# Kernel tuning notes

Hardware: AMD Instinct MI355X
Metric: run time of the kernel (lower is better)

Reference implementation:

```python
import jax, jax.numpy as jnp
import numpy as np

NUM_GROUPS = 32
EPS = 1e-6


def group_norm(x, w, b):
    # x: (B, C, L); normalize per group of C//32 channels over (channels-in-group, L)
    B, C, L = x.shape
    xg = x.reshape(B, NUM_GROUPS, C // NUM_GROUPS, L)
    mean = jnp.mean(xg, axis=(2, 3), keepdims=True)
    var = jnp.var(xg, axis=(2, 3), keepdims=True)
    xn = ((xg - mean) * jax.lax.rsqrt(var + EPS)).reshape(B, C, L)
    return xn * w[None, :, None] + b[None, :, None]


def conv1x1(x, w, b):
    # 1x1 Conv1d == channel-mixing linear. x: (B,C,L), w: (O,C), b: (O,)
    return jnp.einsum('oc,bcl->bol', w, x) + b[None, :, None]


def setup_inputs() -> dict:
    key = jax.random.key(0)
    ks = jax.random.split(key, 6)
    B, C, L = 8, 512, 2048
    s = 1.0 / np.sqrt(C)
    return {
        'x': jax.random.normal(ks[0], (B, C, L), dtype=jnp.float32),
        'gn_w': jnp.ones((C,), jnp.float32),
        'gn_b': jnp.zeros((C,), jnp.float32),
        'wq': jax.random.normal(ks[1], (C, C), dtype=jnp.float32) * s,
        'bq': jnp.zeros((C,), jnp.float32),
        'wk': jax.random.normal(ks[2], (C, C), dtype=jnp.float32) * s,
        'bk': jnp.zeros((C,), jnp.float32),
        'wv': jax.random.normal(ks[3], (C, C), dtype=jnp.float32) * s,
        'bv': jnp.zeros((C,), jnp.float32),
        'wo': jax.random.normal(ks[4], (C, C), dtype=jnp.float32) * s,
        'bo': jnp.zeros((C,), jnp.float32),
    }


def reference(x, gn_w, gn_b, wq, bq, wk, bk, wv, bv, wo, bo):
    B, C, L = x.shape
    h = group_norm(x, gn_w, gn_b)
    q = conv1x1(h, wq, bq)  # (B,C,L)
    k = conv1x1(h, wk, bk)
    v = conv1x1(h, wv, bv)
    scale = jnp.asarray(C, x.dtype) ** -0.5
    # scores over length: w[b,i,j] = sum_c q[b,c,i] k[b,c,j]
    w_ = jnp.einsum('bci,bcj->bij', q, k) * scale
    w_ = jax.nn.softmax(w_, axis=-1)
    # h[b,c,i] = sum_j w[b,i,j] v[b,c,j]
    h = jnp.einsum('bij,bcj->bci', w_, v)
    h = conv1x1(h, wo, bo)
    return x + h
```

## Files before the change

kernel.cpp:

```cpp
#include <hip/hip_runtime.h>
#include <math.h>

#define BATCH 8
#define CH 512
#define LEN 2048
#define NG 32
#define CPG 16

typedef unsigned short u16;
typedef __bf16 bf16x8 __attribute__((ext_vector_type(8)));
typedef float f32x16 __attribute__((ext_vector_type(16)));

__device__ __forceinline__ u16 f2bf(float f) {
    union { float f; unsigned u; } c; c.f = f;
    unsigned r = c.u + 0x7fffu + ((c.u >> 16) & 1u);
    return (u16)(r >> 16);
}
__device__ __forceinline__ float bf2f(u16 h) {
    union { unsigned u; float f; } c; c.u = ((unsigned)h) << 16;
    return c.f;
}
__device__ __forceinline__ void gload16(const u16* g, u16* l) {
    __builtin_amdgcn_global_load_lds(
        (const __attribute__((address_space(1))) unsigned int*)g,
        (__attribute__((address_space(3))) unsigned int*)l, 16, 0, 0);
}

__global__ __launch_bounds__(256) void zerof4(float4* __restrict__ p) {
    p[blockIdx.x * 256 + threadIdx.x] = make_float4(0.f, 0.f, 0.f, 0.f);
}

__global__ __launch_bounds__(256) void wconv4(const float* __restrict__ w0, const float* __restrict__ w1,
                                              const float* __restrict__ w2, const float* __restrict__ w3,
                                              u16* __restrict__ o0, u16* __restrict__ o1,
                                              u16* __restrict__ o2, u16* __restrict__ o3) {
    const float* s; u16* d;
    switch (blockIdx.y) {
        case 0: s = w0; d = o0; break;
        case 1: s = w1; d = o1; break;
        case 2: s = w2; d = o2; break;
        default: s = w3; d = o3; break;
    }
    const int i = blockIdx.x * 256 + threadIdx.x;
    float4 f = ((const float4*)s)[i];
    ushort4 o = make_ushort4(f2bf(f.x), f2bf(f.y), f2bf(f.z), f2bf(f.w));
    ((ushort4*)d)[i] = o;
}

__global__ __launch_bounds__(256) void gn_stats(const float* __restrict__ x,
                                                const float* __restrict__ gw,
                                                const float* __restrict__ gb,
                                                float* __restrict__ gnA,
                                                float* __restrict__ gnB) {
    const int b = blockIdx.x >> 5, g = blockIdx.x & 31;
    const float4* xp = (const float4*)(x + ((size_t)b * CH + (size_t)g * CPG) * LEN);
    float s = 0.f, s2 = 0.f;
    for (int i = threadIdx.x; i < (CPG * LEN) / 4; i += 256) {
        float4 v = xp[i];
        s += v.x + v.y + v.z + v.w;
        s2 = fmaf(v.x, v.x, fmaf(v.y, v.y, fmaf(v.z, v.z, fmaf(v.w, v.w, s2))));
    }
    #pragma unroll
    for (int off = 32; off > 0; off >>= 1) {
        s  += __shfl_down(s, off, 64);
        s2 += __shfl_down(s2, off, 64);
    }
    __shared__ float sm[2][4];
    const int lane = threadIdx.x & 63, wv = threadIdx.x >> 6;
    if (lane == 0) { sm[0][wv] = s; sm[1][wv] = s2; }
    __syncthreads();
    if (threadIdx.x < CPG) {
        const float S  = sm[0][0] + sm[0][1] + sm[0][2] + sm[0][3];
        const float S2 = sm[1][0] + sm[1][1] + sm[1][2] + sm[1][3];
        const float mean = S * (1.f / (CPG * LEN));
        const float var  = S2 * (1.f / (CPG * LEN)) - mean * mean;
        const float rstd = rsqrtf(var + 1e-6f);
        const int c = g * CPG + threadIdx.x;
        const float sc = rstd * gw[c];
        gnA[b * CH + c] = sc;
        gnB[b * CH + c] = gb[c] - mean * sc;
    }
}

__global__ __launch_bounds__(256) void gn_apply_t(const float* __restrict__ x,
                                                  const float* __restrict__ gnA,
                                                  const float* __restrict__ gnB,
                                                  u16* __restrict__ Ht) {
    __shared__ float tile[64][65];
    const int b = blockIdx.z, c0 = blockIdx.y * 64, l0 = blockIdx.x * 64;
    const int t = threadIdx.x, tl = t & 63, tr = t >> 6;
    #pragma unroll 4
    for (int i = 0; i < 16; ++i) {
        const int c = tr + i * 4;
        const float a = gnA[b * CH + c0 + c];
        const float sh = gnB[b * CH + c0 + c];
        tile[c][tl] = x[((size_t)b * CH + c0 + c) * LEN + l0 + tl] * a + sh;
    }
    __syncthreads();
    #pragma unroll 4
    for (int i = 0; i < 16; ++i) {
        const int l = tr + i * 4;
        Ht[((size_t)b * LEN + l0 + l) * CH + c0 + tl] = f2bf(tile[tl][l]);
    }
}

#define EPI_QK   0
#define EPI_TBN  1
#define EPI_EXP  2
#define EPI_TNRM 3
#define EPI_FIN  4

template <int MODE>
__global__ __launch_bounds__(256) void gemm_bt(
    const u16* __restrict__ A, int lda, long long sA,
    const u16* __restrict__ B, int ldb, long long sB,
    void* __restrict__ Out, void* __restrict__ Out2,
    int ldo, long long sO,
    const float* __restrict__ bias, const float* __restrict__ bias2,
    const float* __restrict__ res, long long sR,
    float* __restrict__ rsum, long long sRS,
    int K, float alpha) {
    __shared__ u16 As[128 * 64];
    __shared__ u16 Bs[128 * 64];
    const int b = blockIdx.z;
    const int n0 = blockIdx.x * 128, m0 = blockIdx.y * 128;
    A += (size_t)b * sA;
    B += (size_t)b * sB;
    const int t = threadIdx.x;
    const int lane = t & 63, wid = t >> 6;

    const int rowL = t >> 3, kq = (t & 7) ^ (rowL & 7);
    const u16* gA[4];
    const u16* gB[4];
    u16* lA[4];
    u16* lB[4];
    #pragma unroll
    for (int g = 0; g < 4; ++g) {
        gA[g] = A + (size_t)(m0 + rowL + g * 32) * lda + kq * 8;
        gB[g] = B + (size_t)(n0 + rowL + g * 32) * ldb + kq * 8;
        lA[g] = As + t * 8 + g * 2048;
        lB[g] = Bs + t * 8 + g * 2048;
    }

    f32x16 acc[2][2];
    #pragma unroll
    for (int i = 0; i < 2; ++i)
        #pragma unroll
        for (int j = 0; j < 2; ++j)
            acc[i][j] = (f32x16)(0.f);

    const int col = lane & 31, half = lane >> 5;
    const int wm = (wid & 1) * 64, wn = (wid >> 1) * 64;
    const int mf = wm + col, nf = wn + col;
    const int mswz = mf & 7, nswz = nf & 7;

    for (int k0 = 0; k0 < K; k0 += 64) {
        #pragma unroll
        for (int g = 0; g < 4; ++g) {
            gload16(gA[g], lA[g]);
            gload16(gB[g], lB[g]);
            gA[g] += 64; gB[g] += 64;
        }
        __syncthreads();
        #pragma unroll
        for (int ks = 0; ks < 4; ++ks) {
            const int kcA = ((ks * 2 + half) ^ mswz) * 8;
            const int kcB = ((ks * 2 + half) ^ nswz) * 8;
            bf16x8 a0 = *(const bf16x8*)(As + (mf)      * 64 + kcA);
            bf16x8 a1 = *(const bf16x8*)(As + (mf + 32) * 64 + kcA);
            bf16x8 b0 = *(const bf16x8*)(Bs + (nf)      * 64 + kcB);
            bf16x8 b1 = *(const bf16x8*)(Bs + (nf + 32) * 64 + kcB);
            acc[0][0] = __builtin_amdgcn_mfma_f32_32x32x16_bf16(a0, b0, acc[0][0], 0, 0, 0);
            acc[0][1] = __builtin_amdgcn_mfma_f32_32x32x16_bf16(a0, b1, acc[0][1], 0, 0, 0);
            acc[1][0] = __builtin_amdgcn_mfma_f32_32x32x16_bf16(a1, b0, acc[1][0], 0, 0, 0);
            acc[1][1] = __builtin_amdgcn_mfma_f32_32x32x16_bf16(a1, b1, acc[1][1], 0, 0, 0);
        }
        __syncthreads();
    }

    if (MODE == EPI_FIN) {
        float* O = (float*)Out + (size_t)b * sO;
        const float* R = res + (size_t)b * sR;
        #pragma unroll
        for (int im = 0; im < 2; ++im)
            #pragma unroll
            for (int g4 = 0; g4 < 4; ++g4) {
                const int mb = m0 + wm + im * 32 + g4 * 8 + half * 4;
                #pragma unroll
                for (int jn = 0; jn < 2; ++jn) {
                    const int n = n0 + wn + jn * 32 + col;
                    const float bb = bias[n];
                    const size_t base = (size_t)n * ldo + mb;
                    const float4 r4 = *(const float4*)&R[base];
                    float4 o4;
                    o4.x = acc[im][jn][g4 * 4 + 0] + bb + r4.x;
                    o4.y = acc[im][jn][g4 * 4 + 1] + bb + r4.y;
                    o4.z = acc[im][jn][g4 * 4 + 2] + bb + r4.z;
                    o4.w = acc[im][jn][g4 * 4 + 3] + bb + r4.w;
                    *(float4*)&O[base] = o4;
                }
            }
    } else if (MODE == EPI_EXP) {
        u16* O = (u16*)Out + (size_t)b * sO;
        float* RS = rsum + (size_t)b * sRS;
        float psum[2] = {0.f, 0.f};
        #pragma unroll
        for (int im = 0; im < 2; ++im)
            #pragma unroll
            for (int g4 = 0; g4 < 4; ++g4) {
                const int mb = m0 + wm + im * 32 + g4 * 8 + half * 4;
                #pragma unroll
                for (int jn = 0; jn < 2; ++jn) {
                    const int n = n0 + wn + jn * 32 + col;
                    u16 h0 = f2bf(__expf(acc[im][jn][g4 * 4 + 0] * alpha));
                    u16 h1 = f2bf(__expf(acc[im][jn][g4 * 4 + 1] * alpha));
                    u16 h2 = f2bf(__expf(acc[im][jn][g4 * 4 + 2] * alpha));
                    u16 h3 = f2bf(__expf(acc[im][jn][g4 * 4 + 3] * alpha));
                    psum[jn] += bf2f(h0) + bf2f(h1) + bf2f(h2) + bf2f(h3);
                    *(ushort4*)&O[(size_t)n * ldo + mb] = make_ushort4(h0, h1, h2, h3);
                }
            }
        #pragma unroll
        for (int jn = 0; jn < 2; ++jn) psum[jn] += __shfl_xor(psum[jn], 32, 64);
        if (half == 0) {
            #pragma unroll
            for (int jn = 0; jn < 2; ++jn)
                atomicAdd(&RS[n0 + wn + jn * 32 + col], psum[jn]);
        }
    } else {
        u16* O;
        const float* bi = bias;
        const float* RS = (MODE == EPI_TNRM) ? rsum + (size_t)b * sRS : nullptr;
        int mbase = m0 + wm;
        if (MODE == EPI_QK) {
            const bool hi = (m0 & 512) != 0;
            O  = (u16*)(hi ? Out2 : Out) + (size_t)b * sO;
            bi = hi ? bias2 : bias;
            mbase = (m0 & 511) + wm;
        } else {
            O = (u16*)Out + (size_t)b * sO;
        }
        float inv[2];
        if (MODE == EPI_TNRM) {
            inv[0] = 1.f / RS[n0 + wn + col];
            inv[1] = 1.f / RS[n0 + wn + 32 + col];
        }
        #pragma unroll
        for (int im = 0; im < 2; ++im)
            #pragma unroll
            for (int g4 = 0; g4 < 4; ++g4) {
                const int mb = mbase + im * 32 + g4 * 8 + half * 4;
                float4 bm = make_float4(0.f, 0.f, 0.f, 0.f);
                if (MODE == EPI_QK) bm = *(const float4*)&bi[mb];
                #pragma unroll
                for (int jn = 0; jn < 2; ++jn) {
                    const int n = n0 + wn + jn * 32 + col;
                    float v0 = acc[im][jn][g4 * 4 + 0];
                    float v1 = acc[im][jn][g4 * 4 + 1];
                    float v2 = acc[im][jn][g4 * 4 + 2];
                    float v3 = acc[im][jn][g4 * 4 + 3];
                    if (MODE == EPI_QK)  { v0 += bm.x; v1 += bm.y; v2 += bm.z; v3 += bm.w; }
                    if (MODE == EPI_TBN) { const float bb = bi[n]; v0 += bb; v1 += bb; v2 += bb; v3 += bb; }
                    if (MODE == EPI_TNRM) { v0 *= inv[jn]; v1 *= inv[jn]; v2 *= inv[jn]; v3 *= inv[jn]; }
                    ushort4 pk = make_ushort4(f2bf(v0), f2bf(v1), f2bf(v2), f2bf(v3));
                    *(ushort4*)&O[(size_t)n * ldo + mb] = pk;
                }
            }
    }
}

extern "C" void kernel_launch(void* const* d_in, const int* in_sizes, int n_in,
                              void* d_out, int out_size, void* d_ws, size_t ws_size,
                              hipStream_t stream) {
    const float* x    = (const float*)d_in[0];
    const float* gn_w = (const float*)d_in[1];
    const float* gn_b = (const float*)d_in[2];
    const float* wq   = (const float*)d_in[3];
    const float* bq   = (const float*)d_in[4];
    const float* wk   = (const float*)d_in[5];
    const float* bk   = (const float*)d_in[6];
    const float* wv   = (const float*)d_in[7];
    const float* bv   = (const float*)d_in[8];
    const float* wo   = (const float*)d_in[9];
    const float* bo   = (const float*)d_in[10];
    float* out = (float*)d_out;

    char* p = (char*)d_ws;
    const size_t WSZ = (size_t)CH * CH * 2;
    const size_t HSZ = (size_t)BATCH * CH * LEN * 2;
    u16* Wqk = (u16*)p; p += 2 * WSZ;
    u16* Wvb = (u16*)p; p += WSZ;
    u16* Wob = (u16*)p; p += WSZ;
    u16* Ht  = (u16*)p; p += HSZ;
    u16* Qt  = (u16*)p; p += HSZ;
    u16* Kt  = (u16*)p; p += HSZ;
    u16* Vb  = (u16*)p; p += HSZ;
    u16* Sb  = (u16*)p; p += (size_t)BATCH * LEN * LEN * 2;
    float* gnA = (float*)p; p += (size_t)BATCH * CH * 4;
    float* gnB = (float*)p; p += (size_t)BATCH * CH * 4;
    float* rowsum = (float*)p;

    const long long sH = (long long)LEN * CH;
    const long long sV = (long long)CH * LEN;
    const long long sS = (long long)LEN * LEN;
    const float scale = 0.04419417382415922f;

    wconv4<<<dim3(256, 4), 256, 0, stream>>>(wq, wk, wv, wo,
                                             Wqk, Wqk + (size_t)CH * CH, Wvb, Wob);
    gn_stats<<<BATCH * NG, 256, 0, stream>>>(x, gn_w, gn_b, gnA, gnB);
    gn_apply_t<<<dim3(LEN / 64, CH / 64, BATCH), 256, 0, stream>>>(x, gnA, gnB, Ht);
    zerof4<<<BATCH * LEN / 1024, 256, 0, stream>>>((float4*)rowsum);

    gemm_bt<EPI_QK><<<dim3(16, 8, 8), 256, 0, stream>>>(
        Wqk, CH, 0, Ht, CH, sH, Qt, Kt, CH, sH, bq, bk, nullptr, 0, nullptr, 0, CH, 0.f);
    gemm_bt<EPI_TBN><<<dim3(4, 16, 8), 256, 0, stream>>>(
        Ht, CH, sH, Wvb, CH, 0, Vb, nullptr, LEN, sV, bv, nullptr, nullptr, 0, nullptr, 0, CH, 0.f);
    gemm_bt<EPI_EXP><<<dim3(16, 16, 8), 256, 0, stream>>>(
        Kt, CH, sH, Qt, CH, sH, Sb, nullptr, LEN, sS, nullptr, nullptr, nullptr, 0, rowsum, LEN, CH, scale);
    gemm_bt<EPI_TNRM><<<dim3(16, 4, 8), 256, 0, stream>>>(
        Vb, LEN, sV, Sb, LEN, sS, Ht, nullptr, CH, sH, nullptr, nullptr, nullptr, 0, rowsum, LEN, LEN, 0.f);
    gemm_bt<EPI_FIN><<<dim3(4, 16, 8), 256, 0, stream>>>(
        Ht, CH, sH, Wob, CH, 0, out, nullptr, LEN, sV, bo, nullptr, x, sV, nullptr, 0, CH, 0.f);
}
```

Baseline: 299.2 us.

## Replace 128x128 GEMM with double-buffered 256-wide tiles, 8 waves, XCD-aware block remap

Rewrites the shared GEMM kernel to use 512-thread blocks with BMx256 tiles (BM 128 or 256). LDS is double-buffered so the next K-slice is prefetched with global_load_lds while MFMAs run on the current one, and s_setprio is raised around the MFMA bursts. Block indices are permuted round-robin across 8 groups to spread work over the XCDs. Larger tiles raise per-block LDS and register use and cut the number of blocks, which risks lower occupancy and tail imbalance on some of the GEMMs.

```diff
diff --git a/kernel.cpp b/kernel.cpp
--- a/kernel.cpp
+++ b/kernel.cpp
@@ -25,6 +25,12 @@
         (const __attribute__((address_space(1))) unsigned int*)g,
         (__attribute__((address_space(3))) unsigned int*)l, 16, 0, 0);
 }
+
+#define BARRIER() do {                                   \
+    asm volatile("" ::: "memory");                       \
+    __builtin_amdgcn_s_barrier();                        \
+    asm volatile("" ::: "memory");                       \
+} while (0)
 
 __global__ __launch_bounds__(256) void zerof4(float4* __restrict__ p) {
     p[blockIdx.x * 256 + threadIdx.x] = make_float4(0.f, 0.f, 0.f, 0.f);
@@ -110,8 +116,8 @@
 #define EPI_TNRM 3
 #define EPI_FIN  4
 
-template <int MODE>
-__global__ __launch_bounds__(256) void gemm_bt(
+template <int MODE, int BM>
+__global__ __launch_bounds__(512, 2) void gemm256(
     const u16* __restrict__ A, int lda, long long sA,
     const u16* __restrict__ B, int ldb, long long sB,
     void* __restrict__ Out, void* __restrict__ Out2,
@@ -120,69 +126,116 @@
     const float* __restrict__ res, long long sR,
     float* __restrict__ rsum, long long sRS,
     int K, float alpha) {
-    __shared__ u16 As[128 * 64];
-    __shared__ u16 Bs[128 * 64];
-    const int b = blockIdx.z;
-    const int n0 = blockIdx.x * 128, m0 = blockIdx.y * 128;
-    A += (size_t)b * sA;
-    B += (size_t)b * sB;
+    constexpr int MF = BM / 64;
+    constexpr int RA = BM / 64;
+    __shared__ u16 As[2][BM * 64];
+    __shared__ u16 Bs[2][256 * 64];
+
+    const int gx = gridDim.x, gy = gridDim.y;
+    int flat = (blockIdx.z * gy + blockIdx.y) * gx + blockIdx.x;
+    const int nb = gx * gy * (int)gridDim.z;
+    flat = (flat & 7) * (nb >> 3) + (flat >> 3);
+    const int bz = flat / (gx * gy);
+    const int rr = flat - bz * gx * gy;
+    const int by = rr / gx;
+    const int bx = rr - by * gx;
+
+    const int n0 = bx * 256, m0 = by * BM;
+    A += (size_t)bz * sA;
+    B += (size_t)bz * sB;
+
     const int t = threadIdx.x;
     const int lane = t & 63, wid = t >> 6;
-
-    const int rowL = t >> 3, kq = (t & 7) ^ (rowL & 7);
-    const u16* gA[4];
+    const int col = lane & 31, half = lane >> 5;
+    const int wm = (wid >> 2) * (BM / 2), wn = (wid & 3) * 64;
+
+    const int rowL = t >> 3;
+    const int kq = ((t & 7) ^ (rowL & 7)) * 8;
+    const u16* gA[RA];
     const u16* gB[4];
-    u16* lA[4];
-    u16* lB[4];
-    #pragma unroll
-    for (int g = 0; g < 4; ++g) {
-        gA[g] = A + (size_t)(m0 + rowL + g * 32) * lda + kq * 8;
-        gB[g] = B + (size_t)(n0 + rowL + g * 32) * ldb + kq * 8;
-        lA[g] = As + t * 8 + g * 2048;
-        lB[g] = Bs + t * 8 + g * 2048;
-    }
-
-    f32x16 acc[2][2];
-    #pragma unroll
-    for (int i = 0; i < 2; ++i)
-        #pragma unroll
-        for (int j = 0; j < 2; ++j)
-            acc[i][j] = (f32x16)(0.f);
-
-    const int col = lane & 31, half = lane >> 5;
-    const int wm = (wid & 1) * 64, wn = (wid >> 1) * 64;
-    const int mf = wm + col, nf = wn + col;
-    const int mswz = mf & 7, nswz = nf & 7;
-
-    for (int k0 = 0; k0 < K; k0 += 64) {
-        #pragma unroll
-        for (int g = 0; g < 4; ++g) {
-            gload16(gA[g], lA[g]);
-            gload16(gB[g], lB[g]);
-            gA[g] += 64; gB[g] += 64;
+    #pragma unroll
+    for (int r = 0; r < RA; ++r) gA[r] = A + (size_t)(m0 + r * 64 + rowL) * lda + kq;
+    #pragma unroll
+    for (int r = 0; r < 4; ++r)  gB[r] = B + (size_t)(n0 + r * 64 + rowL) * ldb + kq;
+    const int dst = t * 8;
+
+    f32x16 acc[MF][2];
+    #pragma unroll
+    for (int mi = 0; mi < MF; ++mi)
+        #pragma unroll
+        for (int nj = 0; nj < 2; ++nj)
+            acc[mi][nj] = (f32x16)(0.f);
+
+    #pragma unroll
+    for (int r = 0; r < RA; ++r) { gload16(gA[r], &As[0][r * 4096 + dst]); gA[r] += 64; }
+    #pragma unroll
+    for (int r = 0; r < 4; ++r)  { gload16(gB[r], &Bs[0][r * 4096 + dst]); gB[r] += 64; }
+    asm volatile("s_waitcnt vmcnt(0)" ::: "memory");
+    BARRIER();
+
+    const int NT = K >> 6;
+    const int cw8 = col & 7;
+
+    for (int kt = 0; kt < NT; ++kt) {
+        const int cur = kt & 1;
+        const u16* __restrict__ Ab = As[cur];
+        const u16* __restrict__ Bb = Bs[cur];
+        u16* Ad = As[cur ^ 1];
+        u16* Bd = Bs[cur ^ 1];
+        const bool pf = (kt + 1 < NT);
+
+        #pragma unroll
+        for (int p = 0; p < 2; ++p) {
+            const int s0 = ((4 * p + half) ^ cw8) * 8;
+            const int s1 = ((4 * p + 2 + half) ^ cw8) * 8;
+            bf16x8 av[MF][2], bv[2][2];
+            #pragma unroll
+            for (int mi = 0; mi < MF; ++mi) {
+                const u16* base = Ab + (wm + mi * 32 + col) * 64;
+                av[mi][0] = *(const bf16x8*)(base + s0);
+                av[mi][1] = *(const bf16x8*)(base + s1);
+            }
+            #pragma unroll
+            for (int nj = 0; nj < 2; ++nj) {
+                const u16* base = Bb + (wn + nj * 32 + col) * 64;
+                bv[nj][0] = *(const bf16x8*)(base + s0);
+                bv[nj][1] = *(const bf16x8*)(base + s1);
+            }
+            if (pf) {
+                if (p == 0) {
+                    #pragma unroll
+                    for (int r = 0; r < RA / 2; ++r) { gload16(gA[r], Ad + r * 4096 + dst); gA[r] += 64; }
+                    #pragma unroll
+                    for (int r = 0; r < 2; ++r)      { gload16(gB[r], Bd + r * 4096 + dst); gB[r] += 64; }
+                } else {
+                    #pragma unroll
+                    for (int r = RA / 2; r < RA; ++r) { gload16(gA[r], Ad + r * 4096 + dst); gA[r] += 64; }
+                    #pragma unroll
+                    for (int r = 2; r < 4; ++r)       { gload16(gB[r], Bd + r * 4096 + dst); gB[r] += 64; }
+                }
+            }
+            BARRIER();
+            __builtin_amdgcn_s_setprio(1);
+            #pragma unroll
+            for (int h = 0; h < 2; ++h)
+                #pragma unroll
+                for (int mi = 0; mi < MF; ++mi)
+                    #pragma unroll
+                    for (int nj = 0; nj < 2; ++nj)
+                        acc[mi][nj] = __builtin_amdgcn_mfma_f32_32x32x16_bf16(
+                            av[mi][h], bv[nj][h], acc[mi][nj], 0, 0, 0);
+            __builtin_amdgcn_s_setprio(0);
+            if (p == 0) BARRIER();
         }
-        __syncthreads();
-        #pragma unroll
-        for (int ks = 0; ks < 4; ++ks) {
-            const int kcA = ((ks * 2 + half) ^ mswz) * 8;
-            const int kcB = ((ks * 2 + half) ^ nswz) * 8;
-            bf16x8 a0 = *(const bf16x8*)(As + (mf)      * 64 + kcA);
-            bf16x8 a1 = *(const bf16x8*)(As + (mf + 32) * 64 + kcA);
-            bf16x8 b0 = *(const bf16x8*)(Bs + (nf)      * 64 + kcB);
-            bf16x8 b1 = *(const bf16x8*)(Bs + (nf + 32) * 64 + kcB);
-            acc[0][0] = __builtin_amdgcn_mfma_f32_32x32x16_bf16(a0, b0, acc[0][0], 0, 0, 0);
-            acc[0][1] = __builtin_amdgcn_mfma_f32_32x32x16_bf16(a0, b1, acc[0][1], 0, 0, 0);
-            acc[1][0] = __builtin_amdgcn_mfma_f32_32x32x16_bf16(a1, b0, acc[1][0], 0, 0, 0);
-            acc[1][1] = __builtin_amdgcn_mfma_f32_32x32x16_bf16(a1, b1, acc[1][1], 0, 0, 0);
-        }
-        __syncthreads();
+        asm volatile("s_waitcnt vmcnt(0)" ::: "memory");
+        BARRIER();
     }
 
     if (MODE == EPI_FIN) {
-        float* O = (float*)Out + (size_t)b * sO;
-        const float* R = res + (size_t)b * sR;
-        #pragma unroll
-        for (int im = 0; im < 2; ++im)
+        float* O = (float*)Out + (size_t)bz * sO;
+        const float* R = res + (size_t)bz * sR;
+        #pragma unroll
+        for (int im = 0; im < MF; ++im)
             #pragma unroll
             for (int g4 = 0; g4 < 4; ++g4) {
                 const int mb = m0 + wm + im * 32 + g4 * 8 + half * 4;
@@ -201,11 +254,11 @@
                 }
             }
     } else if (MODE == EPI_EXP) {
-        u16* O = (u16*)Out + (size_t)b * sO;
-        float* RS = rsum + (size_t)b * sRS;
+        u16* O = (u16*)Out + (size_t)bz * sO;
+        float* RS = rsum + (size_t)bz * sRS;
         float psum[2] = {0.f, 0.f};
         #pragma unroll
-        for (int im = 0; im < 2; ++im)
+        for (int im = 0; im < MF; ++im)
             #pragma unroll
             for (int g4 = 0; g4 < 4; ++g4) {
                 const int mb = m0 + wm + im * 32 + g4 * 8 + half * 4;
@@ -230,15 +283,15 @@
     } else {
         u16* O;
         const float* bi = bias;
-        const float* RS = (MODE == EPI_TNRM) ? rsum + (size_t)b * sRS : nullptr;
+        const float* RS = (MODE == EPI_TNRM) ? rsum + (size_t)bz * sRS : nullptr;
         int mbase = m0 + wm;
         if (MODE == EPI_QK) {
             const bool hi = (m0 & 512) != 0;
-            O  = (u16*)(hi ? Out2 : Out) + (size_t)b * sO;
+            O  = (u16*)(hi ? Out2 : Out) + (size_t)bz * sO;
             bi = hi ? bias2 : bias;
             mbase = (m0 & 511) + wm;
         } else {
-            O = (u16*)Out + (size_t)b * sO;
+            O = (u16*)Out + (size_t)bz * sO;
         }
         float inv[2];
         if (MODE == EPI_TNRM) {
@@ -246,7 +299,7 @@
             inv[1] = 1.f / RS[n0 + wn + 32 + col];
         }
         #pragma unroll
-        for (int im = 0; im < 2; ++im)
+        for (int im = 0; im < MF; ++im)
             #pragma unroll
             for (int g4 = 0; g4 < 4; ++g4) {
                 const int mb = mbase + im * 32 + g4 * 8 + half * 4;
@@ -311,14 +364,14 @@
     gn_apply_t<<<dim3(LEN / 64, CH / 64, BATCH), 256, 0, stream>>>(x, gnA, gnB, Ht);
     zerof4<<<BATCH * LEN / 1024, 256, 0, stream>>>((float4*)rowsum);
 
-    gemm_bt<EPI_QK><<<dim3(16, 8, 8), 256, 0, stream>>>(
+    gemm256<EPI_QK, 256><<<dim3(8, 4, 8), 512, 0, stream>>>(
         Wqk, CH, 0, Ht, CH, sH, Qt, Kt, CH, sH, bq, bk, nullptr, 0, nullptr, 0, CH, 0.f);
-    gemm_bt<EPI_TBN><<<dim3(4, 16, 8), 256, 0, stream>>>(
+    gemm256<EPI_TBN, 128><<<dim3(2, 16, 8), 512, 0, stream>>>(
         Ht, CH, sH, Wvb, CH, 0, Vb, nullptr, LEN, sV, bv, nullptr, nullptr, 0, nullptr, 0, CH, 0.f);
-    gemm_bt<EPI_EXP><<<dim3(16, 16, 8), 256, 0, stream>>>(
+    gemm256<EPI_EXP, 256><<<dim3(8, 8, 8), 512, 0, stream>>>(
         Kt, CH, sH, Qt, CH, sH, Sb, nullptr, LEN, sS, nullptr, nullptr, nullptr, 0, rowsum, LEN, CH, scale);
-    gemm_bt<EPI_TNRM><<<dim3(16, 4, 8), 256, 0, stream>>>(
+    gemm256<EPI_TNRM, 128><<<dim3(8, 4, 8), 512, 0, stream>>>(
         Vb, LEN, sV, Sb, LEN, sS, Ht, nullptr, CH, sH, nullptr, nullptr, nullptr, 0, rowsum, LEN, LEN, 0.f);
-    gemm_bt<EPI_FIN><<<dim3(4, 16, 8), 256, 0, stream>>>(
+    gemm256<EPI_FIN, 128><<<dim3(2, 16, 8), 512, 0, stream>>>(
         Ht, CH, sH, Wob, CH, 0, out, nullptr, LEN, sV, bo, nullptr, x, sV, nullptr, 0, CH, 0.f);
 }
```

Measured after the change: 301.5 us. Within noise of the previous version (+0.8%).
